# Optimization experiments

Hardware: AMD Instinct MI355X
Metric: run time of the kernel (lower is better)

Reference implementation:

```python
import jax, jax.numpy as jnp
import numpy as np
from jax import lax

BN_EPS = 1e-5


def _fps(xyz, npoint):
    # Farthest point sampling; deterministic start at index 0 per batch
    # (original uses a random start; the math of the loop is identical).
    B, N, _ = xyz.shape
    init_dist = jnp.full((B, N), 1e10, dtype=xyz.dtype)
    init_far = jnp.zeros((B,), dtype=jnp.int32)

    def step(carry, _):
        dist, far = carry
        centroid = jnp.take_along_axis(xyz, far[:, None, None], axis=1)  # [B,1,3]
        d = jnp.sum((xyz - centroid) ** 2, axis=-1)  # [B,N]
        dist = jnp.minimum(dist, d)
        new_far = jnp.argmax(dist, axis=-1).astype(jnp.int32)
        return (dist, new_far), far

    _, idx = lax.scan(step, (init_dist, init_far), None, length=npoint)
    return jnp.transpose(idx)  # [B, npoint]


def _index_points(points, idx):
    # points [B,N,C], idx [B,...] -> [B,...,C]
    return jax.vmap(lambda p, i: p[i])(points, idx)


def _knn(k, xyz, new_xyz):
    # squared euclidean distances [B,S,N]
    d = (jnp.sum(new_xyz ** 2, -1)[:, :, None]
         + jnp.sum(xyz ** 2, -1)[:, None, :]
         - 2.0 * jnp.einsum('bsc,bnc->bsn', new_xyz, xyz))
    _, idx = lax.top_k(-d, k)  # k smallest distances
    return idx


def _conv_bn_relu(x, w, gamma, beta):
    # 1x1 Conv2d (no bias) + BatchNorm2d (training-mode batch stats) + ReLU
    y = jnp.einsum('oc,bcsk->bosk', w, x)
    mean = jnp.mean(y, axis=(0, 2, 3), keepdims=True)
    var = jnp.var(y, axis=(0, 2, 3), keepdims=True)
    y = (y - mean) * lax.rsqrt(var + BN_EPS)
    y = y * gamma[None, :, None, None] + beta[None, :, None, None]
    return jax.nn.relu(y)


def setup_inputs() -> dict:
    key = jax.random.key(0)
    ks = jax.random.split(key, 5)
    B, N, C = 16, 4096, 128
    xyz = jax.random.normal(ks[0], (B, N, 3), dtype=jnp.float32)
    features = jax.random.normal(ks[1], (B, C, N), dtype=jnp.float32)
    w1 = jax.random.normal(ks[2], (128, C + 3), dtype=jnp.float32) * 0.05
    w2 = jax.random.normal(ks[3], (128, 128), dtype=jnp.float32) * 0.05
    w3 = jax.random.normal(ks[4], (256, 128), dtype=jnp.float32) * 0.05
    return {
        'xyz': xyz, 'features': features,
        'w1': w1, 'g1': jnp.ones(128), 'b1': jnp.zeros(128),
        'w2': w2, 'g2': jnp.ones(128), 'b2': jnp.zeros(128),
        'w3': w3, 'g3': jnp.ones(256), 'b3': jnp.zeros(256),
        'npoint': 1024, 'k': 32,
    }


def reference(xyz, features, w1, g1, b1, w2, g2, b2, w3, g3, b3, npoint, k):
    fps_idx = _fps(xyz, npoint)                     # [B,S]
    new_xyz = _index_points(xyz, fps_idx)           # [B,S,3]
    group_idx = _knn(k, xyz, new_xyz)               # [B,S,K]
    grouped_xyz = _index_points(xyz, group_idx)     # [B,S,K,3]
    gxn = grouped_xyz - new_xyz[:, :, None, :]
    feats = jnp.transpose(features, (0, 2, 1))      # [B,N,C]
    gfeat = _index_points(feats, group_idx)         # [B,S,K,C]
    grouped = jnp.concatenate([gxn, gfeat], axis=-1)  # [B,S,K,3+C]
    x = jnp.transpose(grouped, (0, 3, 1, 2))        # [B,3+C,S,K]
    x = _conv_bn_relu(x, w1, g1, b1)
    x = _conv_bn_relu(x, w2, g2, b2)
    x = _conv_bn_relu(x, w3, g3, b3)
    new_features = jnp.max(x, axis=-1)              # [B,256,S]
    return new_xyz, new_features
```

## Files before the change

kernel.cpp:

```cpp
#include <hip/hip_runtime.h>

#define HB 16
#define HN 4096
#define HS 1024
#define HK 32
#define HC 128
#define NCOL (HB*HS*HK)

typedef _Float16 half8  __attribute__((ext_vector_type(8)));
typedef _Float16 half4v __attribute__((ext_vector_type(4)));
typedef float    f32x4  __attribute__((ext_vector_type(4)));
typedef float    f32x2  __attribute__((ext_vector_type(2)));
typedef unsigned long long u64;

#define WS_STATS   0u
#define WS_BN      4096u
#define WS_A1H     8192u
#define WS_A2H     49152u
#define WS_A3H     81920u
#define WS_XYZPP   147456u
#define WS_GIDX    1196032u
#define WS_FEATT   3293184u
#define WS_Y1      20070400u

__global__ __launch_bounds__(256) void head_kernel(
    const float* __restrict__ xyz, const float* __restrict__ features,
    const float* __restrict__ w1, const float* __restrict__ w2, const float* __restrict__ w3,
    _Float16* __restrict__ a1h, _Float16* __restrict__ a2h, _Float16* __restrict__ a3h,
    _Float16* __restrict__ featt, float4* __restrict__ xyzpp, float* __restrict__ out)
{
#pragma clang fp contract(off)
  __shared__ union {
    float tbuf[64][65];
    struct { uint4 A[2][4]; unsigned Z[2][4]; } fps;
  } lds;
  const int bid = blockIdx.x;
  const int t = threadIdx.x;

  if (bid < 16) {
    const int b = bid;
    const float* xb = xyz + (size_t)b*HN*3;
    f32x2 pX[8], pY[8], pZ[8], dm[8];
    #pragma unroll
    for (int h = 0; h < 8; ++h) {
      #pragma unroll
      for (int e = 0; e < 2; ++e) {
        int n = t*16 + h*2 + e;
        pX[h][e] = xb[n*3+0]; pY[h][e] = xb[n*3+1]; pZ[h][e] = xb[n*3+2];
      }
      dm[h] = f32x2{1e10f, 1e10f};
    }
    float cx = xb[0], cy = xb[1], cz = xb[2];
    float sc[4][3];
    #pragma unroll
    for (int k = 0; k < 4; ++k) { sc[k][0]=0.0f; sc[k][1]=0.0f; sc[k][2]=0.0f; }
    if (t == 0) { out[(size_t)(b*HS)*3+0] = cx; out[(size_t)(b*HS)*3+1] = cy; out[(size_t)(b*HS)*3+2] = cz; }
    const int wv = t >> 6, l = t & 63;

    for (int i = 1; i < HS; ++i) {
      f32x2 vcx = {cx, cx}, vcy = {cy, cy}, vcz = {cz, cz};
      float pm[8];
      #pragma unroll
      for (int h = 0; h < 8; ++h) {
        f32x2 dx = pX[h] - vcx, dy = pY[h] - vcy, dz = pZ[h] - vcz;
        f32x2 d = ((dx*dx) + (dy*dy)) + (dz*dz);
        f32x2 nd = __builtin_elementwise_min(dm[h], d);
        dm[h] = nd;
        pm[h] = fmaxf(nd[0], nd[1]);
      }
      float q0 = fmaxf(pm[0], pm[1]), q1 = fmaxf(pm[2], pm[3]);
      float q2 = fmaxf(pm[4], pm[5]), q3 = fmaxf(pm[6], pm[7]);
      float val = fmaxf(fmaxf(q0, q1), fmaxf(q2, q3));
      int nkey = 0;
      float bx = pX[0][0], by = pY[0][0], bz = pZ[0][0];
      #pragma unroll
      for (int h = 7; h >= 0; --h) {
        bool m0 = (dm[h][0] == val);
        bool m1 = (dm[h][1] == val);
        if (m0 | m1) {
          int e = m0 ? 0 : 1;
          nkey = t*16 + 2*h + e;
          bx = m0 ? pX[h][0] : pX[h][1];
          by = m0 ? pY[h][0] : pY[h][1];
          bz = m0 ? pZ[h][0] : pZ[h][1];
        }
      }
      int ikhi = (int)__float_as_uint(val);
      int iklo = HN-1 - nkey;
      #define TSTEP(ctrl) { \
        int nh_ = __builtin_amdgcn_update_dpp(ikhi, ikhi, ctrl, 0xF, 0xF, false); \
        int nl_ = __builtin_amdgcn_update_dpp(iklo, iklo, ctrl, 0xF, 0xF, false); \
        bool g_ = ((unsigned)nh_ > (unsigned)ikhi) || ((nh_ == ikhi) && (nl_ > iklo)); \
        ikhi = g_ ? nh_ : ikhi; iklo = g_ ? nl_ : iklo; }
      TSTEP(0x111) TSTEP(0x112) TSTEP(0x114) TSTEP(0x118) TSTEP(0x142) TSTEP(0x143)
      #undef TSTEP
      unsigned wkhi = (unsigned)__builtin_amdgcn_readlane(ikhi, 63);
      int wklo = __builtin_amdgcn_readlane(iklo, 63);
      int n_w = HN-1 - wklo;
      int wlane = n_w >> 4;
      float wx = __int_as_float(__builtin_amdgcn_readlane(__float_as_int(bx), wlane));
      float wy = __int_as_float(__builtin_amdgcn_readlane(__float_as_int(by), wlane));
      float wz = __int_as_float(__builtin_amdgcn_readlane(__float_as_int(bz), wlane));

      const int p = i & 1;
      if (l == 0) {
        lds.fps.A[p][wv] = uint4{wkhi, (unsigned)wklo, __float_as_uint(wx), __float_as_uint(wy)};
        lds.fps.Z[p][wv] = __float_as_uint(wz);
      }
      __syncthreads();
      uint4 A0 = lds.fps.A[p][0];
      uint4 A1 = lds.fps.A[p][1];
      uint4 A2 = lds.fps.A[p][2];
      uint4 A3 = lds.fps.A[p][3];
      uint4 Zv = *(const uint4*)&lds.fps.Z[p][0];
      u64 k0 = ((u64)A0.x << 32) | A0.y;
      u64 k1 = ((u64)A1.x << 32) | A1.y;
      u64 k2 = ((u64)A2.x << 32) | A2.y;
      u64 k3 = ((u64)A3.x << 32) | A3.y;
      u64 kA = k0; unsigned xA = A0.z, yA = A0.w, zA = Zv.x;
      if (k1 > kA) { kA = k1; xA = A1.z; yA = A1.w; zA = Zv.y; }
      u64 kB = k2; unsigned xB = A2.z, yB = A2.w, zB = Zv.z;
      if (k3 > kB) { kB = k3; xB = A3.z; yB = A3.w; zB = Zv.w; }
      if (kB > kA) { kA = kB; xA = xB; yA = yB; zA = zB; }
      cx = __uint_as_float(xA); cy = __uint_as_float(yA); cz = __uint_as_float(zA);
      if ((i & 255) == t) {
        int s = i >> 8;
        #pragma unroll
        for (int k = 0; k < 4; ++k)
          if (s == k) { sc[k][0] = cx; sc[k][1] = cy; sc[k][2] = cz; }
      }
    }
    #pragma unroll
    for (int k = 0; k < 4; ++k) {
      int i = k*256 + t;
      if (i >= 1) {
        size_t o3 = (size_t)(b*HS + i)*3;
        out[o3+0] = sc[k][0]; out[o3+1] = sc[k][1]; out[o3+2] = sc[k][2];
      }
    }
  } else if (bid < 16 + 1024) {
    const int tb = bid - 16;
    const int bb = tb >> 6, n0 = (tb & 63) * 64;
    const int wvv = t >> 6, lane = t & 63;
    for (int h = 0; h < 2; ++h) {
      #pragma unroll
      for (int rep = 0; rep < 16; ++rep) {
        int cc = rep*4 + wvv;
        lds.tbuf[cc][lane] = features[((size_t)(bb*HC + h*64 + cc))*HN + n0 + lane];
      }
      __syncthreads();
      #pragma unroll
      for (int rep = 0; rep < 2; ++rep) {
        int item = rep*256 + t;
        int n = item >> 3, cg = (item & 7) * 8;
        half8 v;
        #pragma unroll
        for (int j = 0; j < 8; ++j) v[j] = (_Float16)lds.tbuf[cg + j][n];
        *(half8*)(featt + ((size_t)(bb*HN) + n0 + n) * HC + h*64 + cg) = v;
      }
      __syncthreads();
    }
  } else if (bid < 16 + 1024 + 256) {
    int gi = (bid - 1040)*256 + t;
    const float* p = xyz + (size_t)gi*3;
    float x = p[0], y = p[1], z = p[2];
    float pp = ((x*x) + (y*y)) + (z*z);
    xyzpp[gi] = make_float4(x, y, z, pp);
  } else {
    int wi = (bid - 1296)*256 + t;
    if (wi < 20480) {
      int o = wi / 160, c = wi - o*160;
      float v = 0.0f;
      if (c < 128) v = w1[o*131 + 3 + c];
      else if (c < 131) v = w1[o*131 + (c-128)];
      a1h[wi] = (_Float16)v;
    } else if (wi < 20480 + 16384) {
      a2h[wi - 20480] = (_Float16)w2[wi - 20480];
    } else if (wi < 20480 + 16384 + 32768) {
      a3h[wi - 36864] = (_Float16)w3[wi - 36864];
    }
  }
}

#define LEXLT(d1,i1,d2,i2) ((d1) < (d2) || ((d1) == (d2) && (i1) < (i2)))

__global__ __launch_bounds__(64) void knn_p1(
    const float* __restrict__ newxyz, const float4* __restrict__ xyzpp, u64* __restrict__ keybuf)
{
#pragma clang fp contract(off)
  const int t = threadIdx.x;
  const int blk = blockIdx.x;
  const int b = blk >> 7, rem = blk & 127;
  const int shard = rem >> 4, qg = rem & 15;
  const int q = b*1024 + qg*64 + t;
  float qx = newxyz[(size_t)q*3+0], qy = newxyz[(size_t)q*3+1], qz = newxyz[(size_t)q*3+2];
  float qq = ((qx*qx) + (qy*qy)) + (qz*qz);

  const float INF = __builtin_inff();
  float td[32]; int ti[32];
  #pragma unroll
  for (int j = 0; j < 32; ++j) { td[j] = INF; ti[j] = 0x7FFFFFFF; }
  float root = INF;
  int cnt = 0;

  __shared__ float fdl[32][64];
  __shared__ int   fil[32][64];
  const float4* P = xyzpp + (size_t)b*HN + shard*512;

  auto flush = [&]() {
    float gd[32]; int gi2[32];
    #pragma unroll
    for (int j = 0; j < 32; ++j) {
      gd[j] = fdl[j][t]; gi2[j] = fil[j][t];
      if (j >= cnt) { gd[j] = INF; gi2[j] = 0x7FFFFFFF; }
    }
    cnt = 0;
    #pragma unroll
    for (int k = 2; k <= 32; k <<= 1) {
      #pragma unroll
      for (int j = k >> 1; j > 0; j >>= 1) {
        #pragma unroll
        for (int i = 0; i < 32; ++i) {
          int l = i ^ j;
          if (l > i) {
            bool up = ((i & k) == 0);
            bool sw = up ? LEXLT(gd[l], gi2[l], gd[i], gi2[i])
                         : LEXLT(gd[i], gi2[i], gd[l], gi2[l]);
            if (sw) { float tf = gd[i]; gd[i] = gd[l]; gd[l] = tf;
                      int   ii = gi2[i]; gi2[i] = gi2[l]; gi2[l] = ii; }
          }
        }
      }
    }
    #pragma unroll
    for (int i = 0; i < 32; ++i) {
      float od = gd[31-i]; int oi = gi2[31-i];
      if (LEXLT(od, oi, td[i], ti[i])) { td[i] = od; ti[i] = oi; }
    }
    #pragma unroll
    for (int j = 16; j > 0; j >>= 1) {
      #pragma unroll
      for (int i = 0; i < 32; ++i) {
        if ((i & j) == 0) {
          int l = i | j;
          if (LEXLT(td[l], ti[l], td[i], ti[i])) {
            float tf = td[i]; td[i] = td[l]; td[l] = tf;
            int   ii = ti[i]; ti[i] = ti[l]; ti[l] = ii;
          }
        }
      }
    }
    root = td[31];
  };

  for (int n0 = 0; n0 < 512; n0 += 8) {
    float4 pb[8];
    #pragma unroll
    for (int j = 0; j < 8; ++j) pb[j] = P[n0 + j];
    #pragma unroll
    for (int j = 0; j < 8; ++j) {
      float d = (qq + pb[j].w) - 2.0f*(((qx*pb[j].x) + (qy*pb[j].y)) + (qz*pb[j].z));
      if (d < root) { fdl[cnt][t] = d; fil[cnt][t] = shard*512 + n0 + j; cnt++; }
    }
    if (__ballot(cnt > 24)) flush();
  }
  if (__ballot(cnt > 0)) flush();

  const size_t base = (size_t)(b*16 + qg) * 16384 + (size_t)shard * 2048;
  #pragma unroll
  for (int j = 0; j < 32; ++j) {
    unsigned bits = __float_as_uint(td[j]);
    unsigned s = bits ^ (((unsigned)((int)bits >> 31)) | 0x80000000u);
    keybuf[base + (size_t)j*64 + t] = ((u64)s << 32) | (unsigned)ti[j];
  }
}

__global__ __launch_bounds__(64) void knn_p2(const u64* __restrict__ keybuf, int* __restrict__ gidx)
{
  const int t = threadIdx.x;
  const int g = blockIdx.x;
  const size_t base = (size_t)g * 16384;

  u64 tk[32];
  #pragma unroll
  for (int j = 0; j < 32; ++j) tk[j] = ~0ULL;
  u64 root = ~0ULL;
  int cnt = 0;
  __shared__ u64 fk[32][64];

  auto flush64 = [&]() {
    u64 gd[32];
    #pragma unroll
    for (int j = 0; j < 32; ++j) {
      gd[j] = fk[j][t];
      if (j >= cnt) gd[j] = ~0ULL;
    }
    cnt = 0;
    #pragma unroll
    for (int k = 2; k <= 32; k <<= 1) {
      #pragma unroll
      for (int j = k >> 1; j > 0; j >>= 1) {
        #pragma unroll
        for (int i = 0; i < 32; ++i) {
          int l = i ^ j;
          if (l > i) {
            bool up = ((i & k) == 0);
            bool sw = up ? (gd[l] < gd[i]) : (gd[i] < gd[l]);
            if (sw) { u64 tf = gd[i]; gd[i] = gd[l]; gd[l] = tf; }
          }
        }
      }
    }
    #pragma unroll
    for (int i = 0; i < 32; ++i) {
      u64 od = gd[31-i];
      if (od < tk[i]) tk[i] = od;
    }
    #pragma unroll
    for (int j = 16; j > 0; j >>= 1) {
      #pragma unroll
      for (int i = 0; i < 32; ++i) {
        if ((i & j) == 0) {
          int l = i | j;
          if (tk[l] < tk[i]) { u64 tf = tk[i]; tk[i] = tk[l]; tk[l] = tf; }
        }
      }
    }
    root = tk[31];
  };

  for (int k0 = 0; k0 < 256; k0 += 8) {
    u64 kk[8];
    #pragma unroll
    for (int j = 0; j < 8; ++j) kk[j] = keybuf[base + (size_t)(k0 + j)*64 + t];
    #pragma unroll
    for (int j = 0; j < 8; ++j) {
      if (kk[j] < root) { fk[cnt][t] = kk[j]; cnt++; }
    }
    if (__ballot(cnt > 24)) flush64();
  }
  if (__ballot(cnt > 0)) flush64();

  const int q = g*64 + t;
  #pragma unroll
  for (int j = 0; j < 32; j += 4) {
    int4 v = { (int)(unsigned)tk[j], (int)(unsigned)tk[j+1], (int)(unsigned)tk[j+2], (int)(unsigned)tk[j+3] };
    *(int4*)(gidx + ((size_t)q << 5) + j) = v;
  }
}

template<int MODE>
__global__ __launch_bounds__(256, 2) void conv_kernel(
    const _Float16* __restrict__ A, const _Float16* Bsrc,
    const int* __restrict__ gidx, const float4* __restrict__ xyzpp, const float* __restrict__ newxyz,
    const _Float16* __restrict__ bnA, const _Float16* __restrict__ bnB,
    _Float16* Yout, float* __restrict__ osum, float* __restrict__ osq,
    float* __restrict__ pool)
{
  const int tid = threadIdx.x;
  const int w = tid >> 6, l = tid & 63, ll = l & 15, lh = l >> 4;
  const int colbase = blockIdx.x * 256 + w * 64;
  const int b = colbase >> 15;
  const int AS = (MODE == 1) ? 160 : 128;
  const _Float16* Ap = A + (MODE == 3 ? (size_t)blockIdx.y * 128 * 128 : 0);

  f32x4 acc[8][4] = {};

  half8 bnAv[4], bnBv[4];
  if constexpr (MODE >= 2) {
    #pragma unroll
    for (int c = 0; c < 4; ++c) {
      int k0 = c*32 + lh*8;
      bnAv[c] = *(const half8*)(bnA + k0);
      bnBv[c] = *(const half8*)(bnB + k0);
    }
  }
  int gidxv[4];
  if constexpr (MODE == 1) {
    #pragma unroll
    for (int nf = 0; nf < 4; ++nf) gidxv[nf] = gidx[colbase + nf*16 + ll];
  }

  const int NCH = (MODE == 1) ? 5 : 4;
  #pragma unroll
  for (int c = 0; c < NCH; ++c) {
    half8 a[8];
    #pragma unroll
    for (int mf = 0; mf < 8; ++mf)
      a[mf] = *(const half8*)(Ap + (size_t)(mf*16 + ll)*AS + c*32 + lh*8);
    half8 bfr[4];
    #pragma unroll
    for (int nf = 0; nf < 4; ++nf) {
      if constexpr (MODE == 1) {
        if (c < 4) {
          bfr[nf] = *(const half8*)(Bsrc + ((size_t)(b*HN + gidxv[nf]))*HC + c*32 + lh*8);
        } else {
          half8 z = {};
          if (lh == 0) {
            float4 pw = xyzpp[b*HN + gidxv[nf]];
            int col = colbase + nf*16 + ll;
            int s = (col >> 5) & (HS-1);
            const float* nx = newxyz + (size_t)(b*HS + s)*3;
            z[0] = (_Float16)(pw.x - nx[0]);
            z[1] = (_Float16)(pw.y - nx[1]);
            z[2] = (_Float16)(pw.z - nx[2]);
          }
          bfr[nf] = z;
        }
      } else {
        half8 v = *(const half8*)(Bsrc + ((size_t)(colbase + nf*16 + ll))*HC + c*32 + lh*8);
        v = v * bnAv[c] + bnBv[c];
        half8 hz = {};
        bfr[nf] = __builtin_elementwise_max(v, hz);
      }
    }
    #pragma unroll
    for (int mf = 0; mf < 8; ++mf)
      #pragma unroll
      for (int nf = 0; nf < 4; ++nf)
        acc[mf][nf] = __builtin_amdgcn_mfma_f32_16x16x32_f16(a[mf], bfr[nf], acc[mf][nf], 0, 0, 0);
  }

  __shared__ float bsum[128], bsq[128];
  if (tid < 128) { bsum[tid] = 0.0f; bsq[tid] = 0.0f; }
  __syncthreads();

  #pragma unroll
  for (int mf = 0; mf < 8; ++mf) {
    int ch0 = mf*16 + lh*4;
    if constexpr (MODE != 3) {
      #pragma unroll
      for (int nf = 0; nf < 4; ++nf) {
        int col = colbase + nf*16 + ll;
        half4v hv;
        #pragma unroll
        for (int r = 0; r < 4; ++r) hv[r] = (_Float16)acc[mf][nf][r];
        *(half4v*)(Yout + (size_t)col*HC + ch0) = hv;
      }
    } else {
      #pragma unroll
      for (int g = 0; g < 2; ++g) {
        float mx[4];
        #pragma unroll
        for (int r = 0; r < 4; ++r) mx[r] = fmaxf(acc[mf][2*g][r], acc[mf][2*g+1][r]);
        #pragma unroll
        for (int m = 1; m <= 8; m <<= 1)
          #pragma unroll
          for (int r = 0; r < 4; ++r) mx[r] = fmaxf(mx[r], __shfl_xor(mx[r], m, 64));
        if (ll == 0) {
          int s = ((colbase + g*32) >> 5) & (HS-1);
          int chg = blockIdx.y*128 + ch0;
          #pragma unroll
          for (int r = 0; r < 4; ++r)
            pool[(((size_t)(b*256 + chg + r)) << 10) + s] = mx[r];
        }
      }
    }
    float sv[4] = {0,0,0,0}, qv[4] = {0,0,0,0};
    #pragma unroll
    for (int nf = 0; nf < 4; ++nf)
      #pragma unroll
      for (int r = 0; r < 4; ++r) { float v = acc[mf][nf][r]; sv[r] += v; qv[r] += v*v; }
    #pragma unroll
    for (int m = 1; m <= 8; m <<= 1)
      #pragma unroll
      for (int r = 0; r < 4; ++r) { sv[r] += __shfl_xor(sv[r], m, 64); qv[r] += __shfl_xor(qv[r], m, 64); }
    if (ll == 0) {
      #pragma unroll
      for (int r = 0; r < 4; ++r) { atomicAdd(&bsum[ch0+r], sv[r]); atomicAdd(&bsq[ch0+r], qv[r]); }
    }
  }
  __syncthreads();
  if (tid < 128) {
    int choff = (MODE == 3) ? blockIdx.y*128 : 0;
    atomicAdd(&osum[choff + tid], bsum[tid]);
    atomicAdd(&osq[choff + tid], bsq[tid]);
  }
}

__global__ void fin_kernel(const float* __restrict__ sum, const float* __restrict__ sq,
                           const float* __restrict__ g, const float* __restrict__ be,
                           _Float16* __restrict__ Ah, _Float16* __restrict__ Bh,
                           float* __restrict__ Af, float* __restrict__ Bf, int C)
{
  int c = threadIdx.x;
  if (c < C) {
    float mean = sum[c] * (1.0f/524288.0f);
    float var  = sq[c]  * (1.0f/524288.0f) - mean*mean;
    float a  = g[c] * rsqrtf(var + 1e-5f);
    float bb = be[c] - mean*a;
    if (Ah) { Ah[c] = (_Float16)a; Bh[c] = (_Float16)bb; }
    else    { Af[c] = a; Bf[c] = bb; }
  }
}

__global__ __launch_bounds__(256) void final_affine(float* __restrict__ outp,
                                                    const float* __restrict__ Af,
                                                    const float* __restrict__ Bf)
{
  int i = blockIdx.x*256 + threadIdx.x;
  float4 v = ((float4*)outp)[i];
  int ch = ((i << 2) >> 10) & 255;
  float a = Af[ch], bb = Bf[ch];
  v.x = fmaxf(v.x*a + bb, 0.0f);
  v.y = fmaxf(v.y*a + bb, 0.0f);
  v.z = fmaxf(v.z*a + bb, 0.0f);
  v.w = fmaxf(v.w*a + bb, 0.0f);
  ((float4*)outp)[i] = v;
}

extern "C" void kernel_launch(void* const* d_in, const int* in_sizes, int n_in,
                              void* d_out, int out_size, void* d_ws, size_t ws_size,
                              hipStream_t stream) {
  const float* xyz      = (const float*)d_in[0];
  const float* features = (const float*)d_in[1];
  const float* w1  = (const float*)d_in[2];
  const float* g1  = (const float*)d_in[3];
  const float* b1v = (const float*)d_in[4];
  const float* w2  = (const float*)d_in[5];
  const float* g2  = (const float*)d_in[6];
  const float* b2v = (const float*)d_in[7];
  const float* w3  = (const float*)d_in[8];
  const float* g3  = (const float*)d_in[9];
  const float* b3v = (const float*)d_in[10];
  float* out = (float*)d_out;
  char* ws = (char*)d_ws;

  float* stats = (float*)(ws + WS_STATS);
  float* sum1 = stats;       float* sq1 = stats + 128;
  float* sum2 = stats + 256; float* sq2 = stats + 384;
  float* sum3 = stats + 512; float* sq3 = stats + 768;
  _Float16* A1h = (_Float16*)(ws + WS_BN);
  _Float16* B1h = A1h + 128;
  _Float16* A2h = A1h + 256;
  _Float16* B2h = A1h + 384;
  float* a3f = (float*)(ws + WS_BN + 1024);
  float* b3f = a3f + 256;
  _Float16* a1h = (_Float16*)(ws + WS_A1H);
  _Float16* a2h = (_Float16*)(ws + WS_A2H);
  _Float16* a3h = (_Float16*)(ws + WS_A3H);
  float4* xyzpp = (float4*)(ws + WS_XYZPP);
  int* gidx = (int*)(ws + WS_GIDX);
  _Float16* featt = (_Float16*)(ws + WS_FEATT);
  u64* keybuf = (u64*)(ws + WS_Y1);
  _Float16* y1 = (_Float16*)(ws + WS_Y1);
  _Float16* y2 = y1;

  hipMemsetAsync(ws + WS_STATS, 0, 4096, stream);

  head_kernel<<<1568, 256, 0, stream>>>(xyz, features, w1, w2, w3,
                                        a1h, a2h, a3h, featt, xyzpp, out);
  knn_p1<<<2048, 64, 0, stream>>>(out, xyzpp, keybuf);
  knn_p2<<<256, 64, 0, stream>>>(keybuf, gidx);

  conv_kernel<1><<<2048, 256, 0, stream>>>(a1h, featt, gidx, xyzpp, out,
                                           nullptr, nullptr, y1, sum1, sq1, nullptr);
  fin_kernel<<<1, 256, 0, stream>>>(sum1, sq1, g1, b1v, A1h, B1h, nullptr, nullptr, 128);

  conv_kernel<2><<<2048, 256, 0, stream>>>(a2h, y1, nullptr, nullptr, nullptr,
                                           A1h, B1h, y2, sum2, sq2, nullptr);
  fin_kernel<<<1, 256, 0, stream>>>(sum2, sq2, g2, b2v, A2h, B2h, nullptr, nullptr, 128);

  conv_kernel<3><<<dim3(2048, 2), 256, 0, stream>>>(a3h, y2, nullptr, nullptr, nullptr,
                                                    A2h, B2h, nullptr, sum3, sq3, out + 49152);
  fin_kernel<<<1, 256, 0, stream>>>(sum3, sq3, g3, b3v, nullptr, nullptr, a3f, b3f, 256);

  final_affine<<<4096, 256, 0, stream>>>(out + 49152, a3f, b3f);
}
```

Baseline: 1.635 ms.

## Simplify FPS argmax, halve conv tile width, fuse BN finalize via last-block counter

The FPS loop now reduces only the distance maximum with DPP, picks the winning lane by ballot, and reads the centroid coordinates from an LDS copy of the points, so only a packed 64-bit key is exchanged. The conv kernels process 32 columns per wave instead of 64, doubling the grid and raising the occupancy hint to 3. The separate fin_kernel launches are removed: the last block to finish, detected with an atomic counter, computes the BN scale and shift. This trades fewer launches and registers for more atomics and less reuse of the A fragments per block.

```diff
diff --git a/kernel.cpp b/kernel.cpp
--- a/kernel.cpp
+++ b/kernel.cpp
@@ -15,6 +15,7 @@
 
 #define WS_STATS   0u
 #define WS_BN      4096u
+#define WS_CTR     7168u
 #define WS_A1H     8192u
 #define WS_A2H     49152u
 #define WS_A3H     81920u
@@ -32,7 +33,10 @@
 #pragma clang fp contract(off)
   __shared__ union {
     float tbuf[64][65];
-    struct { uint4 A[2][4]; unsigned Z[2][4]; } fps;
+    struct {
+      float xyzt[HN*3];
+      unsigned long long K[2][4];
+    } fps;
   } lds;
   const int bid = blockIdx.x;
   const int t = threadIdx.x;
@@ -46,7 +50,9 @@
       #pragma unroll
       for (int e = 0; e < 2; ++e) {
         int n = t*16 + h*2 + e;
-        pX[h][e] = xb[n*3+0]; pY[h][e] = xb[n*3+1]; pZ[h][e] = xb[n*3+2];
+        float x = xb[n*3+0], y = xb[n*3+1], z = xb[n*3+2];
+        pX[h][e] = x; pY[h][e] = y; pZ[h][e] = z;
+        lds.fps.xyzt[n*3+0] = x; lds.fps.xyzt[n*3+1] = y; lds.fps.xyzt[n*3+2] = z;
       }
       dm[h] = f32x2{1e10f, 1e10f};
     }
@@ -70,59 +76,45 @@
       }
       float q0 = fmaxf(pm[0], pm[1]), q1 = fmaxf(pm[2], pm[3]);
       float q2 = fmaxf(pm[4], pm[5]), q3 = fmaxf(pm[6], pm[7]);
-      float val = fmaxf(fmaxf(q0, q1), fmaxf(q2, q3));
-      int nkey = 0;
-      float bx = pX[0][0], by = pY[0][0], bz = pZ[0][0];
+      float mymax = fmaxf(fmaxf(q0, q1), fmaxf(q2, q3));
+      int xk = __float_as_int(mymax);
+      #define WMAXSTEP(ctrl) { int o_ = __builtin_amdgcn_update_dpp(xk, xk, ctrl, 0xF, 0xF, false); \
+        xk = __float_as_int(fmaxf(__int_as_float(xk), __int_as_float(o_))); }
+      WMAXSTEP(0x111)
+      WMAXSTEP(0x112)
+      WMAXSTEP(0x114)
+      WMAXSTEP(0x118)
+      WMAXSTEP(0x142)
+      WMAXSTEP(0x143)
+      #undef WMAXSTEP
+      float wmax = __int_as_float(__builtin_amdgcn_readlane(xk, 63));
+      unsigned long long msk = __ballot(mymax == wmax);
+      int winl = __ffsll(msk) - 1;
+      int j = 0;
       #pragma unroll
       for (int h = 7; h >= 0; --h) {
-        bool m0 = (dm[h][0] == val);
-        bool m1 = (dm[h][1] == val);
-        if (m0 | m1) {
-          int e = m0 ? 0 : 1;
-          nkey = t*16 + 2*h + e;
-          bx = m0 ? pX[h][0] : pX[h][1];
-          by = m0 ? pY[h][0] : pY[h][1];
-          bz = m0 ? pZ[h][0] : pZ[h][1];
-        }
-      }
-      int ikhi = (int)__float_as_uint(val);
-      int iklo = HN-1 - nkey;
-      #define TSTEP(ctrl) { \
-        int nh_ = __builtin_amdgcn_update_dpp(ikhi, ikhi, ctrl, 0xF, 0xF, false); \
-        int nl_ = __builtin_amdgcn_update_dpp(iklo, iklo, ctrl, 0xF, 0xF, false); \
-        bool g_ = ((unsigned)nh_ > (unsigned)ikhi) || ((nh_ == ikhi) && (nl_ > iklo)); \
-        ikhi = g_ ? nh_ : ikhi; iklo = g_ ? nl_ : iklo; }
-      TSTEP(0x111) TSTEP(0x112) TSTEP(0x114) TSTEP(0x118) TSTEP(0x142) TSTEP(0x143)
-      #undef TSTEP
-      unsigned wkhi = (unsigned)__builtin_amdgcn_readlane(ikhi, 63);
-      int wklo = __builtin_amdgcn_readlane(iklo, 63);
-      int n_w = HN-1 - wklo;
-      int wlane = n_w >> 4;
-      float wx = __int_as_float(__builtin_amdgcn_readlane(__float_as_int(bx), wlane));
-      float wy = __int_as_float(__builtin_amdgcn_readlane(__float_as_int(by), wlane));
-      float wz = __int_as_float(__builtin_amdgcn_readlane(__float_as_int(bz), wlane));
+        int e = (dm[h][0] == wmax) ? 0 : 1;
+        if (pm[h] == wmax) j = 2*h + e;
+      }
+      int n_cand = t*16 + j;
+      int n_w = __builtin_amdgcn_readlane(n_cand, winl);
 
       const int p = i & 1;
       if (l == 0) {
-        lds.fps.A[p][wv] = uint4{wkhi, (unsigned)wklo, __float_as_uint(wx), __float_as_uint(wy)};
-        lds.fps.Z[p][wv] = __float_as_uint(wz);
+        lds.fps.K[p][wv] = ((unsigned long long)__float_as_uint(wmax) << 32)
+                         | (unsigned int)(HN-1 - n_w);
       }
       __syncthreads();
-      uint4 A0 = lds.fps.A[p][0];
-      uint4 A1 = lds.fps.A[p][1];
-      uint4 A2 = lds.fps.A[p][2];
-      uint4 A3 = lds.fps.A[p][3];
-      uint4 Zv = *(const uint4*)&lds.fps.Z[p][0];
-      u64 k0 = ((u64)A0.x << 32) | A0.y;
-      u64 k1 = ((u64)A1.x << 32) | A1.y;
-      u64 k2 = ((u64)A2.x << 32) | A2.y;
-      u64 k3 = ((u64)A3.x << 32) | A3.y;
-      u64 kA = k0; unsigned xA = A0.z, yA = A0.w, zA = Zv.x;
-      if (k1 > kA) { kA = k1; xA = A1.z; yA = A1.w; zA = Zv.y; }
-      u64 kB = k2; unsigned xB = A2.z, yB = A2.w, zB = Zv.z;
-      if (k3 > kB) { kB = k3; xB = A3.z; yB = A3.w; zB = Zv.w; }
-      if (kB > kA) { kA = kB; xA = xB; yA = yB; zA = zB; }
-      cx = __uint_as_float(xA); cy = __uint_as_float(yA); cz = __uint_as_float(zA);
+      unsigned long long k0 = lds.fps.K[p][0], k1 = lds.fps.K[p][1];
+      unsigned long long k2 = lds.fps.K[p][2], k3 = lds.fps.K[p][3];
+      unsigned long long ka = (k0 >= k1) ? k0 : k1;
+      unsigned long long kb = (k2 >= k3) ? k2 : k3;
+      unsigned long long kk = (ka >= kb) ? ka : kb;
+      int n_best = HN-1 - (int)(unsigned int)(kk & 0xFFFFFFFFull);
+      int off = n_best*3;
+      cx = lds.fps.xyzt[off+0];
+      cy = lds.fps.xyzt[off+1];
+      cz = lds.fps.xyzt[off+2];
       if ((i & 255) == t) {
         int s = i >> 8;
         #pragma unroll
@@ -350,21 +342,24 @@
 }
 
 template<int MODE>
-__global__ __launch_bounds__(256, 2) void conv_kernel(
+__global__ __launch_bounds__(256, 3) void conv_kernel(
     const _Float16* __restrict__ A, const _Float16* Bsrc,
     const int* __restrict__ gidx, const float4* __restrict__ xyzpp, const float* __restrict__ newxyz,
     const _Float16* __restrict__ bnA, const _Float16* __restrict__ bnB,
     _Float16* Yout, float* __restrict__ osum, float* __restrict__ osq,
-    float* __restrict__ pool)
+    float* __restrict__ pool,
+    const float* __restrict__ gg, const float* __restrict__ be,
+    _Float16* Ah, _Float16* Bh, float* Af, float* Bf,
+    unsigned* ctr, unsigned total, int C)
 {
   const int tid = threadIdx.x;
   const int w = tid >> 6, l = tid & 63, ll = l & 15, lh = l >> 4;
-  const int colbase = blockIdx.x * 256 + w * 64;
+  const int colbase = blockIdx.x * 128 + w * 32;
   const int b = colbase >> 15;
   const int AS = (MODE == 1) ? 160 : 128;
   const _Float16* Ap = A + (MODE == 3 ? (size_t)blockIdx.y * 128 * 128 : 0);
 
-  f32x4 acc[8][4] = {};
+  f32x4 acc[8][2] = {};
 
   half8 bnAv[4], bnBv[4];
   if constexpr (MODE >= 2) {
@@ -375,10 +370,10 @@
       bnBv[c] = *(const half8*)(bnB + k0);
     }
   }
-  int gidxv[4];
+  int gidxv[2];
   if constexpr (MODE == 1) {
     #pragma unroll
-    for (int nf = 0; nf < 4; ++nf) gidxv[nf] = gidx[colbase + nf*16 + ll];
+    for (int nf = 0; nf < 2; ++nf) gidxv[nf] = gidx[colbase + nf*16 + ll];
   }
 
   const int NCH = (MODE == 1) ? 5 : 4;
@@ -388,9 +383,9 @@
     #pragma unroll
     for (int mf = 0; mf < 8; ++mf)
       a[mf] = *(const half8*)(Ap + (size_t)(mf*16 + ll)*AS + c*32 + lh*8);
-    half8 bfr[4];
-    #pragma unroll
-    for (int nf = 0; nf < 4; ++nf) {
+    half8 bfr[2];
+    #pragma unroll
+    for (int nf = 0; nf < 2; ++nf) {
       if constexpr (MODE == 1) {
         if (c < 4) {
           bfr[nf] = *(const half8*)(Bsrc + ((size_t)(b*HN + gidxv[nf]))*HC + c*32 + lh*8);
@@ -417,11 +412,12 @@
     #pragma unroll
     for (int mf = 0; mf < 8; ++mf)
       #pragma unroll
-      for (int nf = 0; nf < 4; ++nf)
+      for (int nf = 0; nf < 2; ++nf)
         acc[mf][nf] = __builtin_amdgcn_mfma_f32_16x16x32_f16(a[mf], bfr[nf], acc[mf][nf], 0, 0, 0);
   }
 
   __shared__ float bsum[128], bsq[128];
+  __shared__ unsigned lastf;
   if (tid < 128) { bsum[tid] = 0.0f; bsq[tid] = 0.0f; }
   __syncthreads();
 
@@ -430,7 +426,7 @@
     int ch0 = mf*16 + lh*4;
     if constexpr (MODE != 3) {
       #pragma unroll
-      for (int nf = 0; nf < 4; ++nf) {
+      for (int nf = 0; nf < 2; ++nf) {
         int col = colbase + nf*16 + ll;
         half4v hv;
         #pragma unroll
@@ -438,27 +434,24 @@
         *(half4v*)(Yout + (size_t)col*HC + ch0) = hv;
       }
     } else {
-      #pragma unroll
-      for (int g = 0; g < 2; ++g) {
-        float mx[4];
-        #pragma unroll
-        for (int r = 0; r < 4; ++r) mx[r] = fmaxf(acc[mf][2*g][r], acc[mf][2*g+1][r]);
-        #pragma unroll
-        for (int m = 1; m <= 8; m <<= 1)
-          #pragma unroll
-          for (int r = 0; r < 4; ++r) mx[r] = fmaxf(mx[r], __shfl_xor(mx[r], m, 64));
-        if (ll == 0) {
-          int s = ((colbase + g*32) >> 5) & (HS-1);
-          int chg = blockIdx.y*128 + ch0;
-          #pragma unroll
-          for (int r = 0; r < 4; ++r)
-            pool[(((size_t)(b*256 + chg + r)) << 10) + s] = mx[r];
-        }
+      float mx[4];
+      #pragma unroll
+      for (int r = 0; r < 4; ++r) mx[r] = fmaxf(acc[mf][0][r], acc[mf][1][r]);
+      #pragma unroll
+      for (int m = 1; m <= 8; m <<= 1)
+        #pragma unroll
+        for (int r = 0; r < 4; ++r) mx[r] = fmaxf(mx[r], __shfl_xor(mx[r], m, 64));
+      if (ll == 0) {
+        int s = (colbase >> 5) & (HS-1);
+        int chg = blockIdx.y*128 + ch0;
+        #pragma unroll
+        for (int r = 0; r < 4; ++r)
+          pool[(((size_t)(b*256 + chg + r)) << 10) + s] = mx[r];
       }
     }
     float sv[4] = {0,0,0,0}, qv[4] = {0,0,0,0};
     #pragma unroll
-    for (int nf = 0; nf < 4; ++nf)
+    for (int nf = 0; nf < 2; ++nf)
       #pragma unroll
       for (int r = 0; r < 4; ++r) { float v = acc[mf][nf][r]; sv[r] += v; qv[r] += v*v; }
     #pragma unroll
@@ -476,21 +469,20 @@
     atomicAdd(&osum[choff + tid], bsum[tid]);
     atomicAdd(&osq[choff + tid], bsq[tid]);
   }
-}
-
-__global__ void fin_kernel(const float* __restrict__ sum, const float* __restrict__ sq,
-                           const float* __restrict__ g, const float* __restrict__ be,
-                           _Float16* __restrict__ Ah, _Float16* __restrict__ Bh,
-                           float* __restrict__ Af, float* __restrict__ Bf, int C)
-{
-  int c = threadIdx.x;
-  if (c < C) {
-    float mean = sum[c] * (1.0f/524288.0f);
-    float var  = sq[c]  * (1.0f/524288.0f) - mean*mean;
-    float a  = g[c] * rsqrtf(var + 1e-5f);
-    float bb = be[c] - mean*a;
-    if (Ah) { Ah[c] = (_Float16)a; Bh[c] = (_Float16)bb; }
-    else    { Af[c] = a; Bf[c] = bb; }
+  __threadfence();
+  __syncthreads();
+  if (tid == 0) lastf = (atomicAdd(ctr, 1u) == total - 1u) ? 1u : 0u;
+  __syncthreads();
+  if (lastf && tid < C) {
+    __threadfence();
+    float s  = atomicAdd(&osum[tid], 0.0f);
+    float sq = atomicAdd(&osq[tid], 0.0f);
+    float mean = s  * (1.0f/524288.0f);
+    float var  = sq * (1.0f/524288.0f) - mean*mean;
+    float a  = gg[tid] * rsqrtf(var + 1e-5f);
+    float bb = be[tid] - mean*a;
+    if constexpr (MODE != 3) { Ah[tid] = (_Float16)a; Bh[tid] = (_Float16)bb; }
+    else                     { Af[tid] = a; Bf[tid] = bb; }
   }
 }
 
@@ -536,6 +528,7 @@
   _Float16* B2h = A1h + 384;
   float* a3f = (float*)(ws + WS_BN + 1024);
   float* b3f = a3f + 256;
+  unsigned* ctr = (unsigned*)(ws + WS_CTR);
   _Float16* a1h = (_Float16*)(ws + WS_A1H);
   _Float16* a2h = (_Float16*)(ws + WS_A2H);
   _Float16* a3h = (_Float16*)(ws + WS_A3H);
@@ -546,24 +539,27 @@
   _Float16* y1 = (_Float16*)(ws + WS_Y1);
   _Float16* y2 = y1;
 
-  hipMemsetAsync(ws + WS_STATS, 0, 4096, stream);
+  hipMemsetAsync(ws + WS_STATS, 0, 8192, stream);
 
   head_kernel<<<1568, 256, 0, stream>>>(xyz, features, w1, w2, w3,
                                         a1h, a2h, a3h, featt, xyzpp, out);
   knn_p1<<<2048, 64, 0, stream>>>(out, xyzpp, keybuf);
   knn_p2<<<256, 64, 0, stream>>>(keybuf, gidx);
 
-  conv_kernel<1><<<2048, 256, 0, stream>>>(a1h, featt, gidx, xyzpp, out,
-                                           nullptr, nullptr, y1, sum1, sq1, nullptr);
-  fin_kernel<<<1, 256, 0, stream>>>(sum1, sq1, g1, b1v, A1h, B1h, nullptr, nullptr, 128);
-
-  conv_kernel<2><<<2048, 256, 0, stream>>>(a2h, y1, nullptr, nullptr, nullptr,
-                                           A1h, B1h, y2, sum2, sq2, nullptr);
-  fin_kernel<<<1, 256, 0, stream>>>(sum2, sq2, g2, b2v, A2h, B2h, nullptr, nullptr, 128);
-
-  conv_kernel<3><<<dim3(2048, 2), 256, 0, stream>>>(a3h, y2, nullptr, nullptr, nullptr,
-                                                    A2h, B2h, nullptr, sum3, sq3, out + 49152);
-  fin_kernel<<<1, 256, 0, stream>>>(sum3, sq3, g3, b3v, nullptr, nullptr, a3f, b3f, 256);
+  conv_kernel<1><<<4096, 256, 0, stream>>>(a1h, featt, gidx, xyzpp, out,
+                                           nullptr, nullptr, y1, sum1, sq1, nullptr,
+                                           g1, b1v, A1h, B1h, nullptr, nullptr,
+                                           ctr + 0, 4096u, 128);
+
+  conv_kernel<2><<<4096, 256, 0, stream>>>(a2h, y1, nullptr, nullptr, nullptr,
+                                           A1h, B1h, y2, sum2, sq2, nullptr,
+                                           g2, b2v, A2h, B2h, nullptr, nullptr,
+                                           ctr + 1, 4096u, 128);
+
+  conv_kernel<3><<<dim3(4096, 2), 256, 0, stream>>>(a3h, y2, nullptr, nullptr, nullptr,
+                                                    A2h, B2h, nullptr, sum3, sq3, out + 49152,
+                                                    g3, b3v, nullptr, nullptr, a3f, b3f,
+                                                    ctr + 2, 8192u, 256);
 
   final_affine<<<4096, 256, 0, stream>>>(out + 49152, a3f, b3f);
 }
```

New measurement: 3.445 ms. 2.11x slower.
